# Kernel optimization log

Measured on AMD Instinct MI355X. Metric: run time of the kernel, lower is better.

The kernel has to match this reference:

```python
import jax, jax.numpy as jnp
import numpy as np

EMBED, HID, H = 1024, 1024, 16
D = HID // H
B, L = 4, 4096


def setup_inputs() -> dict:
    key = jax.random.key(0)
    ks = jax.random.split(key, 16)
    s = 0.02
    return {
        "emb": jax.random.normal(ks[0], (B, L, EMBED), jnp.float32),
        "Wa_w": jax.random.normal(ks[1], (HID, EMBED), jnp.float32) * s,
        "Wa_b": jnp.zeros((HID,), jnp.float32),
        "Wb_w": jax.random.normal(ks[2], (HID, EMBED), jnp.float32) * s,
        "Wb_b": jnp.zeros((HID,), jnp.float32),
        "Wo_w": jax.random.normal(ks[3], (HID, EMBED), jnp.float32) * s,
        "Wo_b": jnp.zeros((HID,), jnp.float32),
        "C_w": jax.random.normal(ks[4], (HID, HID), jnp.float32) * s,
        "C_b": jnp.zeros((HID,), jnp.float32),
        "ln_g": jnp.ones((HID,), jnp.float32),
        "ln_b": jnp.zeros((HID,), jnp.float32),
        "f1_w": jax.random.normal(ks[5], (4 * HID, HID), jnp.float32) * s,
        "f1_b": jnp.zeros((4 * HID,), jnp.float32),
        "f2_w": jax.random.normal(ks[6], (HID, 4 * HID), jnp.float32) * s,
        "f2_b": jnp.zeros((HID,), jnp.float32),
        "p_w": jax.random.normal(ks[7], (HID, HID), jnp.float32) * s,
        "p_b": jnp.zeros((HID,), jnp.float32),
        "head_weights": jnp.ones((H,), jnp.float32),
    }


def _layernorm(x, g, b, eps=1e-5):
    mu = jnp.mean(x, axis=-1, keepdims=True)
    var = jnp.mean(jnp.square(x - mu), axis=-1, keepdims=True)
    return (x - mu) * jax.lax.rsqrt(var + eps) * g + b


def _affine_combine(x, y):
    a1, b1 = x
    a2, b2 = y
    return a1 * a2, a2 * b1 + b2


def reference(emb, Wa_w, Wa_b, Wb_w, Wb_b, Wo_w, Wo_b, C_w, C_b, ln_g, ln_b,
              f1_w, f1_b, f2_w, f2_b, p_w, p_b, head_weights):
    Bv, Lv, _ = emb.shape
    a = jnp.tanh(emb @ Wa_w.T + Wa_b).reshape(Bv, Lv, H, D)
    b = (emb @ Wb_w.T + Wb_b).reshape(Bv, Lv, H, D)
    w = (emb @ Wo_w.T + Wo_b).reshape(Bv, Lv, H, D)
    # h_t = a_t * h_{t-1} + b_t, h_0 = 0 -> parallel associative scan over L
    _, h_seq = jax.lax.associative_scan(_affine_combine, (a, b), axis=1)
    # batched per-step C projection over full hidden dim
    c_out = (h_seq.reshape(Bv, Lv, HID) @ C_w.T + C_b).reshape(Bv, Lv, H, D)
    z = (head_weights[None, None, :, None] * (c_out + w)).reshape(Bv, Lv, HID)
    u = z + _layernorm(z, ln_g, ln_b)
    ffn = jax.nn.gelu(u @ f1_w.T + f1_b, approximate=False)
    out = ffn @ f2_w.T + f2_b
    return (u + out) @ p_w.T + p_b
```

## Files before the change

kernel.cpp:

```cpp
#include <hip/hip_runtime.h>
#include <hip/hip_bf16.h>

typedef __attribute__((ext_vector_type(8))) short short8;
typedef __attribute__((ext_vector_type(4))) float f32x4;

#define DEVI static __device__ __forceinline__

constexpr int HID = 1024;
constexpr int BB = 4, LL = 4096;
constexpr int MROWS = BB * LL;
constexpr int NCH = 64, TCH = 64;

constexpr size_t ELN_EMB  = 0;
constexpr size_t ELN_WABO = 16777216;
constexpr size_t ELN_CW   = 19922944;
constexpr size_t ELN_F1   = 20971520;
constexpr size_t ELN_F2   = 25165824;
constexpr size_t ELN_PW   = 29360128;
constexpr size_t ELN_END  = 30408704;
constexpr size_t POOL_BYTES = ELN_END * 2;

constexpr size_t OFF_ABW = POOL_BYTES;
constexpr size_t OFF_H   = OFF_ABW + (size_t)MROWS*3072*2;
constexpr size_t OFF_U   = OFF_H  + (size_t)MROWS*1024*2;
constexpr size_t OFF_AGG = OFF_U  + (size_t)MROWS*1024*2;
constexpr size_t AG_ELEMS = (size_t)BB * NCH * HID;
constexpr size_t WS_NEEDED = OFF_AGG + AG_ELEMS * 4 * 3;

DEVI unsigned short f2b(float x) {
  unsigned u = __float_as_uint(x);
  return (unsigned short)((u + 0x7fffu + ((u >> 16) & 1u)) >> 16);
}
DEVI float b2f(unsigned short u) { return __uint_as_float((unsigned)u << 16); }

DEVI float fast_tanh(float y) {
  y = fminf(fmaxf(y, -10.f), 10.f);
  float e = __expf(2.f * y);
  return (e - 1.f) / (e + 1.f);
}
DEVI float gelu_fast(float x) {
  float t = 0.7978845608028654f * (x + 0.044715f * x * x * x);
  return 0.5f * x * (1.f + fast_tanh(t));
}

DEVI void gload_lds16(const unsigned short* g, unsigned short* l) {
  __builtin_amdgcn_global_load_lds(
      (const __attribute__((address_space(1))) void*)g,
      (__attribute__((address_space(3))) void*)l, 16, 0, 0);
}
DEVI void sbar() { __builtin_amdgcn_s_barrier(); }
DEVI void vmwait0() { asm volatile("s_waitcnt vmcnt(0)" ::: "memory"); }

constexpr long CH_EMB = 16777216 / 8;
constexpr long CH_W   = 1048576 / 8;
constexpr long CH_F   = 4194304 / 8;
constexpr long SEG1 = CH_EMB;
constexpr long SEG2 = SEG1 + CH_W;
constexpr long SEG3 = SEG2 + CH_W;
constexpr long SEG4 = SEG3 + CH_W;
constexpr long SEG5 = SEG4 + CH_W;
constexpr long SEG6 = SEG5 + CH_F;
constexpr long SEG7 = SEG6 + CH_F;
constexpr long SEG8 = SEG7 + CH_W;

__global__ __launch_bounds__(256) void convert_all(
    const float* __restrict__ emb, const float* __restrict__ wa,
    const float* __restrict__ wb,  const float* __restrict__ wo,
    const float* __restrict__ cw,  const float* __restrict__ f1,
    const float* __restrict__ f2,  const float* __restrict__ pw,
    unsigned short* __restrict__ dst) {
  const long stride = (long)gridDim.x * blockDim.x;
  for (long ck = (long)blockIdx.x * blockDim.x + threadIdx.x; ck < SEG8; ck += stride) {
    const float* s; size_t d;
    if (ck < SEG1)      { s = emb + (size_t)ck * 8;        d = ELN_EMB + (size_t)ck * 8; }
    else if (ck < SEG2) { s = wa + (size_t)(ck-SEG1) * 8;  d = ELN_WABO + (size_t)(ck-SEG1) * 8; }
    else if (ck < SEG3) { s = wb + (size_t)(ck-SEG2) * 8;  d = ELN_WABO + 1048576 + (size_t)(ck-SEG2) * 8; }
    else if (ck < SEG4) { s = wo + (size_t)(ck-SEG3) * 8;  d = ELN_WABO + 2097152 + (size_t)(ck-SEG3) * 8; }
    else if (ck < SEG5) { s = cw + (size_t)(ck-SEG4) * 8;  d = ELN_CW + (size_t)(ck-SEG4) * 8; }
    else if (ck < SEG6) { s = f1 + (size_t)(ck-SEG5) * 8;  d = ELN_F1 + (size_t)(ck-SEG5) * 8; }
    else if (ck < SEG7) { s = f2 + (size_t)(ck-SEG6) * 8;  d = ELN_F2 + (size_t)(ck-SEG6) * 8; }
    else                { s = pw + (size_t)(ck-SEG7) * 8;  d = ELN_PW + (size_t)(ck-SEG7) * 8; }
    float4 x = *(const float4*)s;
    float4 y = *(const float4*)(s + 4);
    short8 o;
    o[0]=(short)f2b(x.x); o[1]=(short)f2b(x.y); o[2]=(short)f2b(x.z); o[3]=(short)f2b(x.w);
    o[4]=(short)f2b(y.x); o[5]=(short)f2b(y.y); o[6]=(short)f2b(y.z); o[7]=(short)f2b(y.w);
    *(short8*)(dst + d) = o;
  }
}

template <int EPI>
__global__ __launch_bounds__(512) void gemm256(
    const unsigned short* __restrict__ A, const unsigned short* __restrict__ Bw,
    int K, int NT, int ldo, int addld,
    const float* __restrict__ biasA, const float* __restrict__ biasB,
    const float* __restrict__ biasW,
    const unsigned short* __restrict__ addB, const float* __restrict__ hw,
    float* __restrict__ outF, unsigned short* __restrict__ outB) {
  __shared__ alignas(16) unsigned short lds[2][2][16384];
  const int tid = threadIdx.x;
  const int lane = tid & 63, wave = tid >> 6;
  const int wr = wave >> 2, wc = wave & 3;
  const int arow0 = blockIdx.x * 256, bcol0 = blockIdx.y * 256;
  const int rowb = tid >> 3, kc = (tid & 7) * 8;
  const unsigned short* Ag = A + (size_t)(arow0 + rowb) * K + kc;
  const unsigned short* Bg = Bw + (size_t)(bcol0 + rowb) * K + kc;
  f32x4 acc[8][4] = {};
  const int fm = lane & 15, fg = lane >> 4;

#define STAGE8(p, kt) do { const int k0_ = (kt) * 64;                              \
    _Pragma("unroll") for (int l = 0; l < 4; ++l) {                                \
      gload_lds16(Ag + (size_t)(64 * l) * K + k0_, &lds[p][0][tid * 8 + 4096 * l]);\
      gload_lds16(Bg + (size_t)(64 * l) * K + k0_, &lds[p][1][tid * 8 + 4096 * l]);\
    } } while (0)

  STAGE8(0, 0);
  vmwait0();
  sbar();

  for (int t = 0; t < NT; ++t) {
    const int p = t & 1;
    if (t + 1 < NT) STAGE8(p ^ 1, t + 1);
    const unsigned short* LA = &lds[p][0][(wr * 128 + fm) * 64 + fg * 8];
    const unsigned short* LB = &lds[p][1][(wc * 64 + fm) * 64 + fg * 8];
    short8 af[4], bf[4];
#pragma unroll
    for (int n = 0; n < 4; ++n) bf[n] = *(const short8*)(LB + n * 16 * 64);
#pragma unroll
    for (int m = 0; m < 4; ++m) af[m] = *(const short8*)(LA + m * 16 * 64);
    __builtin_amdgcn_s_setprio(1);
#pragma unroll
    for (int m = 0; m < 4; ++m)
#pragma unroll
      for (int n = 0; n < 4; ++n)
        acc[m][n] = __builtin_amdgcn_mfma_f32_16x16x32_bf16(af[m], bf[n], acc[m][n], 0, 0, 0);
    __builtin_amdgcn_s_setprio(0);
    sbar();
#pragma unroll
    for (int m = 0; m < 4; ++m) af[m] = *(const short8*)(LA + (64 + m * 16) * 64);
    __builtin_amdgcn_s_setprio(1);
#pragma unroll
    for (int m = 0; m < 4; ++m)
#pragma unroll
      for (int n = 0; n < 4; ++n)
        acc[4 + m][n] = __builtin_amdgcn_mfma_f32_16x16x32_bf16(af[m], bf[n], acc[4 + m][n], 0, 0, 0);
    __builtin_amdgcn_s_setprio(0);
    sbar();
#pragma unroll
    for (int n = 0; n < 4; ++n) bf[n] = *(const short8*)(LB + n * 16 * 64 + 32);
#pragma unroll
    for (int m = 0; m < 4; ++m) af[m] = *(const short8*)(LA + m * 16 * 64 + 32);
    __builtin_amdgcn_s_setprio(1);
#pragma unroll
    for (int m = 0; m < 4; ++m)
#pragma unroll
      for (int n = 0; n < 4; ++n)
        acc[m][n] = __builtin_amdgcn_mfma_f32_16x16x32_bf16(af[m], bf[n], acc[m][n], 0, 0, 0);
    __builtin_amdgcn_s_setprio(0);
    sbar();
#pragma unroll
    for (int m = 0; m < 4; ++m) af[m] = *(const short8*)(LA + (64 + m * 16) * 64 + 32);
    __builtin_amdgcn_s_setprio(1);
#pragma unroll
    for (int m = 0; m < 4; ++m)
#pragma unroll
      for (int n = 0; n < 4; ++n)
        acc[4 + m][n] = __builtin_amdgcn_mfma_f32_16x16x32_bf16(af[m], bf[n], acc[4 + m][n], 0, 0, 0);
    __builtin_amdgcn_s_setprio(0);
    vmwait0();
    sbar();
    __builtin_amdgcn_sched_barrier(0);
  }
#undef STAGE8

  const int crow = (lane >> 4) * 4, ccol = lane & 15;
#pragma unroll
  for (int m = 0; m < 8; ++m) {
    const int row0 = arow0 + wr * 128 + (m >> 2) * 64 + (m & 3) * 16 + crow;
#pragma unroll
    for (int n = 0; n < 4; ++n) {
      const int col = bcol0 + wc * 64 + n * 16 + ccol;
#pragma unroll
      for (int r = 0; r < 4; ++r) {
        const size_t orow = (size_t)(row0 + r);
        float x = acc[m][n][r];
        if constexpr (EPI == 0) {
          const int cb = col >> 10;
          const float* bp = (cb == 0) ? biasA : (cb == 1 ? biasB : biasW);
          x += bp[col & 1023];
          if (cb == 0) x = fast_tanh(x);
          outB[orow * 3072 + col] = f2b(x);
        } else if constexpr (EPI == 1) {
          x += biasA[col] + b2f(addB[orow * (size_t)addld + col]);
          x *= hw[col >> 6];
          outB[orow * (size_t)ldo + col] = f2b(x);
        } else if constexpr (EPI == 2) {
          x += biasA[col];
          outB[orow * (size_t)ldo + col] = f2b(gelu_fast(x));
        } else if constexpr (EPI == 3) {
          x += biasA[col] + b2f(addB[orow * (size_t)addld + col]);
          outB[orow * (size_t)ldo + col] = f2b(x);
        } else {
          outF[orow * (size_t)ldo + col] = x + biasA[col];
        }
      }
    }
  }
}

__global__ __launch_bounds__(256) void scan_p1(const unsigned short* __restrict__ abw,
                                               float* __restrict__ agA,
                                               float* __restrict__ agB) {
  const int idx = blockIdx.x;
  const int cg = idx & 3, ch = (idx >> 2) & (NCH - 1), bb = idx >> 8;
  const int c = cg * 256 + threadIdx.x;
  const size_t base = ((size_t)bb * LL + (size_t)ch * TCH) * 3072 + c;
  float A = 1.f, Bg = 0.f;
#pragma unroll 4
  for (int t = 0; t < TCH; ++t) {
    float at = b2f(abw[base + (size_t)t * 3072]);
    float bt = b2f(abw[base + (size_t)t * 3072 + 1024]);
    Bg = fmaf(at, Bg, bt);
    A *= at;
  }
  const size_t o = ((size_t)bb * NCH + ch) * HID + c;
  agA[o] = A;
  agB[o] = Bg;
}

__global__ __launch_bounds__(256) void scan_p2(const float* __restrict__ agA,
                                               const float* __restrict__ agB,
                                               float* __restrict__ pre) {
  const int gid = blockIdx.x * 256 + threadIdx.x;
  const int bb = gid >> 10, c = gid & 1023;
  float h = 0.f;
  for (int ch = 0; ch < NCH; ++ch) {
    const size_t o = ((size_t)bb * NCH + ch) * HID + c;
    pre[o] = h;
    h = fmaf(agA[o], h, agB[o]);
  }
}

__global__ __launch_bounds__(256) void scan_p3(const unsigned short* __restrict__ abw,
                                               const float* __restrict__ pre,
                                               unsigned short* __restrict__ hout) {
  const int idx = blockIdx.x;
  const int cg = idx & 3, ch = (idx >> 2) & (NCH - 1), bb = idx >> 8;
  const int c = cg * 256 + threadIdx.x;
  const size_t base = ((size_t)bb * LL + (size_t)ch * TCH) * 3072 + c;
  const size_t hbase = ((size_t)bb * LL + (size_t)ch * TCH) * HID + c;
  float h = pre[((size_t)bb * NCH + ch) * HID + c];
#pragma unroll 4
  for (int t = 0; t < TCH; ++t) {
    float at = b2f(abw[base + (size_t)t * 3072]);
    float bt = b2f(abw[base + (size_t)t * 3072 + 1024]);
    h = fmaf(at, h, bt);
    hout[hbase + (size_t)t * HID] = f2b(h);
  }
}

__global__ __launch_bounds__(256) void ln_kernel(const unsigned short* __restrict__ abw,
                                                 const float* __restrict__ gam,
                                                 const float* __restrict__ bet,
                                                 unsigned short* __restrict__ u) {
  const int wave = threadIdx.x >> 6, lane = threadIdx.x & 63;
  const int row = blockIdx.x * 4 + wave;
  const unsigned short* zr = abw + (size_t)row * 3072 + lane * 16;
  short8 z0 = *(const short8*)zr;
  short8 z1 = *(const short8*)(zr + 8);
  float x[16];
#pragma unroll
  for (int e = 0; e < 8; ++e) {
    x[e]     = b2f((unsigned short)z0[e]);
    x[8 + e] = b2f((unsigned short)z1[e]);
  }
  float s = 0.f, s2 = 0.f;
#pragma unroll
  for (int e = 0; e < 16; ++e) { s += x[e]; s2 += x[e] * x[e]; }
#pragma unroll
  for (int off = 32; off > 0; off >>= 1) {
    s += __shfl_xor(s, off, 64);
    s2 += __shfl_xor(s2, off, 64);
  }
  const float mu = s * (1.f / 1024.f);
  const float var = s2 * (1.f / 1024.f) - mu * mu;
  const float rs = rsqrtf(var + 1e-5f);
  const float* gp = gam + lane * 16;
  const float* bp = bet + lane * 16;
  short8 o0, o1;
#pragma unroll
  for (int e = 0; e < 8; ++e) {
    float v0 = x[e]     + (x[e]     - mu) * rs * gp[e]     + bp[e];
    float v1 = x[8 + e] + (x[8 + e] - mu) * rs * gp[8 + e] + bp[8 + e];
    o0[e] = (short)f2b(v0);
    o1[e] = (short)f2b(v1);
  }
  unsigned short* ur = u + (size_t)row * HID + lane * 16;
  *(short8*)ur = o0;
  *(short8*)(ur + 8) = o1;
}

extern "C" void kernel_launch(void* const* d_in, const int* in_sizes, int n_in,
                              void* d_out, int out_size, void* d_ws, size_t ws_size,
                              hipStream_t stream) {
  if (ws_size < WS_NEEDED) return;

  const float* emb   = (const float*)d_in[0];
  const float* Wa_w  = (const float*)d_in[1];
  const float* Wa_b  = (const float*)d_in[2];
  const float* Wb_w  = (const float*)d_in[3];
  const float* Wb_b  = (const float*)d_in[4];
  const float* Wo_w  = (const float*)d_in[5];
  const float* Wo_b  = (const float*)d_in[6];
  const float* C_w   = (const float*)d_in[7];
  const float* C_b   = (const float*)d_in[8];
  const float* ln_g  = (const float*)d_in[9];
  const float* ln_b  = (const float*)d_in[10];
  const float* f1_w  = (const float*)d_in[11];
  const float* f1_b  = (const float*)d_in[12];
  const float* f2_w  = (const float*)d_in[13];
  const float* f2_b  = (const float*)d_in[14];
  const float* p_w   = (const float*)d_in[15];
  const float* p_b   = (const float*)d_in[16];
  const float* headw = (const float*)d_in[17];

  char* ws = (char*)d_ws;
  unsigned short* bfp  = (unsigned short*)ws;
  unsigned short* abwB = (unsigned short*)(ws + OFF_ABW);
  unsigned short* hB   = (unsigned short*)(ws + OFF_H);
  unsigned short* uB   = (unsigned short*)(ws + OFF_U);
  unsigned short* ffnB = abwB;
  float* agA = (float*)(ws + OFF_AGG);
  float* agB = agA + AG_ELEMS;
  float* pre = agB + AG_ELEMS;

  convert_all<<<2048, 256, 0, stream>>>(emb, Wa_w, Wb_w, Wo_w, C_w, f1_w, f2_w, p_w, bfp);

  gemm256<0><<<dim3(64, 12), 512, 0, stream>>>(
      bfp + ELN_EMB, bfp + ELN_WABO, 1024, 16, 3072, 0,
      Wa_b, Wb_b, Wo_b, nullptr, nullptr, nullptr, abwB);

  scan_p1<<<BB * NCH * 4, 256, 0, stream>>>(abwB, agA, agB);
  scan_p2<<<16, 256, 0, stream>>>(agA, agB, pre);
  scan_p3<<<BB * NCH * 4, 256, 0, stream>>>(abwB, pre, hB);

  gemm256<1><<<dim3(64, 4), 512, 0, stream>>>(
      hB, bfp + ELN_CW, 1024, 16, 3072, 3072,
      C_b, nullptr, nullptr, abwB + 2048, headw, nullptr, abwB);

  ln_kernel<<<4096, 256, 0, stream>>>(abwB, ln_g, ln_b, uB);

  gemm256<2><<<dim3(64, 16), 512, 0, stream>>>(
      uB, bfp + ELN_F1, 1024, 16, 4096, 0,
      f1_b, nullptr, nullptr, nullptr, nullptr, nullptr, ffnB);

  gemm256<3><<<dim3(64, 4), 512, 0, stream>>>(
      ffnB, bfp + ELN_F2, 4096, 64, 1024, 1024,
      f2_b, nullptr, nullptr, uB, nullptr, nullptr, uB);

  gemm256<4><<<dim3(64, 4), 512, 0, stream>>>(
      uB, bfp + ELN_PW, 1024, 16, 1024, 0,
      p_b, nullptr, nullptr, nullptr, nullptr, (float*)d_out, nullptr);
}
```

Before: 664.0 us.

## Use 4-stage K=32 LDS pipeline with XOR-swizzled A/B tiles in GEMM

Restructures the bf16 GEMM mainloop from a 2-stage double buffer with K=64 tiles into a 4-deep ring of K=32 tiles. Loads for three steps ahead are issued, and only partial vmcnt waits are used, so global-to-LDS transfers overlap more MFMA work. A and B halves now share one LDS stage with an XOR swizzle on the 16-byte chunks, meant to avoid LDS bank conflicts on fragment reads. The cost is twice as many loop iterations and barriers, and vmcnt bookkeeping that must exactly match the number of outstanding loads.

```diff
diff --git a/kernel.cpp b/kernel.cpp
--- a/kernel.cpp
+++ b/kernel.cpp
@@ -49,7 +49,6 @@
       (__attribute__((address_space(3))) void*)l, 16, 0, 0);
 }
 DEVI void sbar() { __builtin_amdgcn_s_barrier(); }
-DEVI void vmwait0() { asm volatile("s_waitcnt vmcnt(0)" ::: "memory"); }
 
 constexpr long CH_EMB = 16777216 / 8;
 constexpr long CH_W   = 1048576 / 8;
@@ -97,37 +96,47 @@
     const float* __restrict__ biasW,
     const unsigned short* __restrict__ addB, const float* __restrict__ hw,
     float* __restrict__ outF, unsigned short* __restrict__ outB) {
-  __shared__ alignas(16) unsigned short lds[2][2][16384];
+  __shared__ alignas(16) unsigned short lds[4][16384];
   const int tid = threadIdx.x;
   const int lane = tid & 63, wave = tid >> 6;
   const int wr = wave >> 2, wc = wave & 3;
   const int arow0 = blockIdx.x * 256, bcol0 = blockIdx.y * 256;
-  const int rowb = tid >> 3, kc = (tid & 7) * 8;
-  const unsigned short* Ag = A + (size_t)(arow0 + rowb) * K + kc;
-  const unsigned short* Bg = Bw + (size_t)(bcol0 + rowb) * K + kc;
   f32x4 acc[8][4] = {};
   const int fm = lane & 15, fg = lane >> 4;
-
-#define STAGE8(p, kt) do { const int k0_ = (kt) * 64;                              \
-    _Pragma("unroll") for (int l = 0; l < 4; ++l) {                                \
-      gload_lds16(Ag + (size_t)(64 * l) * K + k0_, &lds[p][0][tid * 8 + 4096 * l]);\
-      gload_lds16(Bg + (size_t)(64 * l) * K + k0_, &lds[p][1][tid * 8 + 4096 * l]);\
-    } } while (0)
-
-  STAGE8(0, 0);
-  vmwait0();
+  const int sA = (fg ^ (fm & 7)) * 8;
+  const int sB = ((4 + fg) ^ (fm & 7)) * 8;
+
+#define MKSRC(l)                                                                   \
+  const unsigned short* src##l; {                                                  \
+    const int row_ = (tid >> 3) + 64 * l;                                          \
+    const int c_ = (tid & 7) ^ (row_ & 7);                                         \
+    src##l = (c_ < 4) ? A + (size_t)(arow0 + row_) * K + c_ * 8                    \
+                      : Bw + (size_t)(bcol0 + row_) * K + (c_ - 4) * 8; }
+  MKSRC(0) MKSRC(1) MKSRC(2) MKSRC(3)
+#undef MKSRC
+
+#define STAGE(p, t) do { const int ko_ = (t) * 32;                                 \
+    gload_lds16(src0 + ko_, &lds[p][tid * 8]);                                     \
+    gload_lds16(src1 + ko_, &lds[p][tid * 8 + 4096]);                              \
+    gload_lds16(src2 + ko_, &lds[p][tid * 8 + 8192]);                              \
+    gload_lds16(src3 + ko_, &lds[p][tid * 8 + 12288]); } while (0)
+
+  STAGE(0, 0);
+  if (NT > 1) STAGE(1, 1);
+  if (NT > 2) STAGE(2, 2);
+  asm volatile("s_waitcnt vmcnt(8)" ::: "memory");
   sbar();
 
   for (int t = 0; t < NT; ++t) {
-    const int p = t & 1;
-    if (t + 1 < NT) STAGE8(p ^ 1, t + 1);
-    const unsigned short* LA = &lds[p][0][(wr * 128 + fm) * 64 + fg * 8];
-    const unsigned short* LB = &lds[p][1][(wc * 64 + fm) * 64 + fg * 8];
+    const int p = t & 3;
+    const unsigned short* LA = &lds[p][(wr * 128 + fm) * 64];
+    const unsigned short* LB = &lds[p][(wc * 64 + fm) * 64];
     short8 af[4], bf[4];
-#pragma unroll
-    for (int n = 0; n < 4; ++n) bf[n] = *(const short8*)(LB + n * 16 * 64);
-#pragma unroll
-    for (int m = 0; m < 4; ++m) af[m] = *(const short8*)(LA + m * 16 * 64);
+    if (t + 3 < NT) STAGE((t + 3) & 3, t + 3);
+#pragma unroll
+    for (int n = 0; n < 4; ++n) bf[n] = *(const short8*)(LB + n * 1024 + sB);
+#pragma unroll
+    for (int m = 0; m < 4; ++m) af[m] = *(const short8*)(LA + m * 1024 + sA);
     __builtin_amdgcn_s_setprio(1);
 #pragma unroll
     for (int m = 0; m < 4; ++m)
@@ -137,7 +146,7 @@
     __builtin_amdgcn_s_setprio(0);
     sbar();
 #pragma unroll
-    for (int m = 0; m < 4; ++m) af[m] = *(const short8*)(LA + (64 + m * 16) * 64);
+    for (int m = 0; m < 4; ++m) af[m] = *(const short8*)(LA + 4096 + m * 1024 + sA);
     __builtin_amdgcn_s_setprio(1);
 #pragma unroll
     for (int m = 0; m < 4; ++m)
@@ -145,33 +154,14 @@
       for (int n = 0; n < 4; ++n)
         acc[4 + m][n] = __builtin_amdgcn_mfma_f32_16x16x32_bf16(af[m], bf[n], acc[4 + m][n], 0, 0, 0);
     __builtin_amdgcn_s_setprio(0);
-    sbar();
-#pragma unroll
-    for (int n = 0; n < 4; ++n) bf[n] = *(const short8*)(LB + n * 16 * 64 + 32);
-#pragma unroll
-    for (int m = 0; m < 4; ++m) af[m] = *(const short8*)(LA + m * 16 * 64 + 32);
-    __builtin_amdgcn_s_setprio(1);
-#pragma unroll
-    for (int m = 0; m < 4; ++m)
-#pragma unroll
-      for (int n = 0; n < 4; ++n)
-        acc[m][n] = __builtin_amdgcn_mfma_f32_16x16x32_bf16(af[m], bf[n], acc[m][n], 0, 0, 0);
-    __builtin_amdgcn_s_setprio(0);
-    sbar();
-#pragma unroll
-    for (int m = 0; m < 4; ++m) af[m] = *(const short8*)(LA + (64 + m * 16) * 64 + 32);
-    __builtin_amdgcn_s_setprio(1);
-#pragma unroll
-    for (int m = 0; m < 4; ++m)
-#pragma unroll
-      for (int n = 0; n < 4; ++n)
-        acc[4 + m][n] = __builtin_amdgcn_mfma_f32_16x16x32_bf16(af[m], bf[n], acc[4 + m][n], 0, 0, 0);
-    __builtin_amdgcn_s_setprio(0);
-    vmwait0();
+    const int nleft = NT - 2 - t;
+    if (nleft >= 2)      asm volatile("s_waitcnt vmcnt(8)" ::: "memory");
+    else if (nleft == 1) asm volatile("s_waitcnt vmcnt(4)" ::: "memory");
+    else                 asm volatile("s_waitcnt vmcnt(0)" ::: "memory");
     sbar();
     __builtin_amdgcn_sched_barrier(0);
   }
-#undef STAGE8
+#undef STAGE
 
   const int crow = (lane >> 4) * 4, ccol = lane & 15;
 #pragma unroll
@@ -337,7 +327,7 @@
   convert_all<<<2048, 256, 0, stream>>>(emb, Wa_w, Wb_w, Wo_w, C_w, f1_w, f2_w, p_w, bfp);
 
   gemm256<0><<<dim3(64, 12), 512, 0, stream>>>(
-      bfp + ELN_EMB, bfp + ELN_WABO, 1024, 16, 3072, 0,
+      bfp + ELN_EMB, bfp + ELN_WABO, 1024, 32, 3072, 0,
       Wa_b, Wb_b, Wo_b, nullptr, nullptr, nullptr, abwB);
 
   scan_p1<<<BB * NCH * 4, 256, 0, stream>>>(abwB, agA, agB);
@@ -345,20 +335,20 @@
   scan_p3<<<BB * NCH * 4, 256, 0, stream>>>(abwB, pre, hB);
 
   gemm256<1><<<dim3(64, 4), 512, 0, stream>>>(
-      hB, bfp + ELN_CW, 1024, 16, 3072, 3072,
+      hB, bfp + ELN_CW, 1024, 32, 3072, 3072,
       C_b, nullptr, nullptr, abwB + 2048, headw, nullptr, abwB);
 
   ln_kernel<<<4096, 256, 0, stream>>>(abwB, ln_g, ln_b, uB);
 
   gemm256<2><<<dim3(64, 16), 512, 0, stream>>>(
-      uB, bfp + ELN_F1, 1024, 16, 4096, 0,
+      uB, bfp + ELN_F1, 1024, 32, 4096, 0,
       f1_b, nullptr, nullptr, nullptr, nullptr, nullptr, ffnB);
 
   gemm256<3><<<dim3(64, 4), 512, 0, stream>>>(
-      ffnB, bfp + ELN_F2, 4096, 64, 1024, 1024,
+      ffnB, bfp + ELN_F2, 4096, 128, 1024, 1024,
       f2_b, nullptr, nullptr, uB, nullptr, nullptr, uB);
 
   gemm256<4><<<dim3(64, 4), 512, 0, stream>>>(
-      uB, bfp + ELN_PW, 1024, 16, 1024, 0,
+      uB, bfp + ELN_PW, 1024, 32, 1024, 0,
       p_b, nullptr, nullptr, nullptr, nullptr, (float*)d_out, nullptr);
 }
```

Result: faster. 581.9 us (-12.4%).
